# Kernel optimization log

Hardware: AMD Instinct MI355X
Metric: run time of the kernel (lower is better)

The kernel has to match this reference:

```python
import jax, jax.numpy as jnp
import numpy as np

N, H, INTER, M = 8192, 2048, 8192, 2
UP_OUT = 2 * INTER  # gated: up_gate produces interleaved (glu, linear) pairs
EPS = 1e-6
ALPHA = 1.702
LIMIT = 7.0


def setup_inputs() -> dict:
    key = jax.random.key(0)
    k1, k2, k3, k4 = jax.random.split(key, 4)
    x = jax.random.normal(k1, (N, H), dtype=jnp.float32)
    # token stream is pre-permuted so same-modality tokens are contiguous;
    # balanced groups: first N//2 tokens modality 0, rest modality 1
    modality_mapping = jnp.repeat(jnp.arange(M, dtype=jnp.int64), N // M)
    w_norm = jax.random.normal(k2, (H * M,), dtype=jnp.float32) * 0.02
    w_up = jax.random.normal(k3, (UP_OUT * M, H), dtype=jnp.float32) * 0.02
    w_down = jax.random.normal(k4, (H * M, INTER), dtype=jnp.float32) * 0.02
    return {"x": x, "modality_mapping": modality_mapping,
            "w_norm": w_norm, "w_up": w_up, "w_down": w_down}


def reference(x, modality_mapping, w_norm, w_up, w_down):
    # x: [N, H], pre-grouped into M equal contiguous modality chunks.
    n, h = x.shape
    g = n // M  # tokens per modality group
    # ---- MultiModalityRMSNorm (effective weight = 1 + w) ----
    t = x * jax.lax.rsqrt(jnp.mean(x * x, axis=-1, keepdims=True) + EPS)
    tm = t.reshape(M, g, h)                       # [M, g, H]
    tm = tm * (w_norm.reshape(M, 1, h) + 1.0)
    # ---- PackedExpertLinear up_gate: per-modality weight chunk ----
    Wu = w_up.reshape(M, UP_OUT, h)               # [M, 2*INTER, H]
    y = jnp.einsum('mgh,moh->mgo', tm, Wu)        # [M, g, 2*INTER]
    # ---- swiglu7: clamped gated SwiGLU with +1 linear bias ----
    y_glu = jnp.minimum(y[..., ::2], LIMIT)
    y_lin = jnp.clip(y[..., 1::2], -LIMIT, LIMIT)
    a = y_glu * jax.nn.sigmoid(ALPHA * y_glu) * (y_lin + 1.0)  # [M, g, INTER]
    # ---- PackedExpertLinear down_proj ----
    Wd = w_down.reshape(M, h, INTER)              # [M, H, INTER]
    z = jnp.einsum('mgi,mhi->mgh', a, Wd)         # [M, g, H]
    return z.reshape(n, h)
```

## Files before the change

kernel.cpp:

```cpp
#include <hip/hip_runtime.h>
#include <hip/hip_bf16.h>

#define DEVI __device__ __forceinline__

typedef __bf16 bf16x8 __attribute__((ext_vector_type(8)));
typedef float f32x4 __attribute__((ext_vector_type(4)));

namespace {

constexpr int H = 2048;
constexpr int INTER = 8192;
constexpr int M_MOD = 2;
constexpr int N_TOK = 8192;
constexpr int G = N_TOK / M_MOD;
constexpr int UP_OUT = 2 * INTER;

DEVI unsigned short f2bf(float f) {
  unsigned u = __builtin_bit_cast(unsigned, f);
  u += 0x7fffu + ((u >> 16) & 1u);
  return (unsigned short)(u >> 16);
}

DEVI void gload_lds16(const void* g, void* lds) {
  __builtin_amdgcn_global_load_lds(
      (const __attribute__((address_space(1))) unsigned int*)g,
      (__attribute__((address_space(3))) unsigned int*)lds, 16, 0, 0);
}

DEVI void memfence_barrier() {
  asm volatile("" ::: "memory");
  __builtin_amdgcn_s_barrier();
  asm volatile("" ::: "memory");
}

__global__ __launch_bounds__(256) void cvt_f32_bf16(
    const float* __restrict__ in, unsigned short* __restrict__ out, int n4) {
  int idx = blockIdx.x * blockDim.x + threadIdx.x;
  int stride = gridDim.x * blockDim.x;
  for (int i = idx; i < n4; i += stride) {
    float4 v = ((const float4*)in)[i];
    ushort4 o;
    o.x = f2bf(v.x); o.y = f2bf(v.y); o.z = f2bf(v.z); o.w = f2bf(v.w);
    ((ushort4*)out)[i] = o;
  }
}

__global__ __launch_bounds__(256) void rmsnorm_kernel(
    const float* __restrict__ x, const float* __restrict__ w_norm,
    unsigned short* __restrict__ tm) {
  const int row = blockIdx.x;
  const int mod = row >> 12;
  const int t = threadIdx.x;
  const float4* xr = (const float4*)(x + (size_t)row * H);
  const float4* wr = (const float4*)(w_norm + (size_t)mod * H);

  float4 v0 = xr[t];
  float4 v1 = xr[t + 256];
  float ss = v0.x * v0.x + v0.y * v0.y + v0.z * v0.z + v0.w * v0.w +
             v1.x * v1.x + v1.y * v1.y + v1.z * v1.z + v1.w * v1.w;
  #pragma unroll
  for (int o = 32; o > 0; o >>= 1) ss += __shfl_down(ss, o);
  __shared__ float red[4];
  const int w = t >> 6, l = t & 63;
  if (l == 0) red[w] = ss;
  __syncthreads();
  float tot = red[0] + red[1] + red[2] + red[3];
  float rn = rsqrtf(tot * (1.0f / H) + 1e-6f);

  float4 w0 = wr[t];
  float4 w1 = wr[t + 256];
  ushort4 o0, o1;
  o0.x = f2bf(v0.x * rn * (1.f + w0.x));
  o0.y = f2bf(v0.y * rn * (1.f + w0.y));
  o0.z = f2bf(v0.z * rn * (1.f + w0.z));
  o0.w = f2bf(v0.w * rn * (1.f + w0.w));
  o1.x = f2bf(v1.x * rn * (1.f + w1.x));
  o1.y = f2bf(v1.y * rn * (1.f + w1.y));
  o1.z = f2bf(v1.z * rn * (1.f + w1.z));
  o1.w = f2bf(v1.w * rn * (1.f + w1.w));
  ushort4* tr = (ushort4*)(tm + (size_t)row * H);
  tr[t] = o0;
  tr[t + 256] = o1;
}

template <int K, int CT_PER_MOD, int EPI>
__global__ __launch_bounds__(512, 2) void gemm8p(
    const unsigned short* __restrict__ A0, const unsigned short* __restrict__ B0,
    void* __restrict__ O0, long sAm, long sBm, long sOm) {
  __shared__ __align__(16) char smem[2][2][32768];

  constexpr int NT = K / 64;
  constexpr int HMAX = 4 * NT;
  constexpr int NITER = NT / 2;
  constexpr int PER_MOD = 16 * CT_PER_MOD;
  constexpr int NWG = 2 * PER_MOD;
  constexpr int CPX = NWG / 8;

  const int bid0 = blockIdx.x;
  const int bid = (bid0 % 8) * CPX + bid0 / 8;
  const int mod = bid / PER_MOD;
  const int q = bid % PER_MOD;
  const int ct = q / 16;
  const int rt = q % 16;

  const unsigned short* A = A0 + (long)mod * sAm;
  const unsigned short* B = B0 + (long)mod * sBm;

  const int t = threadIdx.x;
  const int w = t >> 6;
  const int l = t & 63;
  const int wr = w >> 2;
  const int wc = w & 3;

  const int fr = l & 15;
  const int fk = l >> 4;
  const int frx = (fr & 7) << 4;

  const unsigned short* gArow = A + (size_t)rt * 256 * K;
  const unsigned short* gBrow = B + (size_t)ct * 256 * K;
  const int srow = t >> 3;
  const int scol = ((t & 7) ^ (srow & 7)) * 8;

  auto stage = [&](int h) {
    if (h >= HMAX) h -= HMAX;
    const int tt = h >> 2, qq = h & 3;
    const int isB = qq >> 1, half = qq & 1, buf = tt & 1;
    const unsigned short* src = (isB ? gBrow : gArow) +
        (size_t)(half * 128 + srow) * K + tt * 64 + scol;
    char* dst = smem[buf][isB] + half * 16384 + t * 16;
    gload_lds16(src, dst);
    gload_lds16(src + (size_t)64 * K, dst + 8192);
  };

  auto rdA = [&](const char* base, int mi, int ks) -> bf16x8 {
    const int row = wr * 128 + mi * 16 + fr;
    return *(const bf16x8*)(base + row * 128 + ((((ks << 2) + fk) << 4) ^ frx));
  };
  auto rdB = [&](const char* base, int ni, int ks) -> bf16x8 {
    const int row = wc * 64 + ni * 16 + fr;
    return *(const bf16x8*)(base + row * 128 + ((((ks << 2) + fk) << 4) ^ frx));
  };

  f32x4 acc[8][4];
  #pragma unroll
  for (int m = 0; m < 8; ++m)
    #pragma unroll
    for (int n = 0; n < 4; ++n) acc[m][n] = (f32x4){0.f, 0.f, 0.f, 0.f};

  bf16x8 a[4][2], b[4][2];

#define MFMAQ(MLO, NLO)                                                       \
  __builtin_amdgcn_s_setprio(1);                                              \
  _Pragma("unroll") for (int ks = 0; ks < 2; ++ks)                            \
  _Pragma("unroll") for (int mi = 0; mi < 4; ++mi)                            \
  _Pragma("unroll") for (int ni = 0; ni < 2; ++ni)                            \
    acc[(MLO) + mi][(NLO) + ni] = __builtin_amdgcn_mfma_f32_16x16x32_bf16(    \
        a[mi][ks], b[(NLO) + ni][ks], acc[(MLO) + mi][(NLO) + ni], 0, 0, 0);  \
  __builtin_amdgcn_s_setprio(0);

  stage(0); stage(1); stage(2); stage(3); stage(4);
  asm volatile("s_waitcnt vmcnt(2)" ::: "memory");
  memfence_barrier();

  const char* A0b = smem[0][0];
  const char* B0b = smem[0][1];
  const char* A1b = smem[1][0];
  const char* B1b = smem[1][1];

  for (int i = 0; i < NITER; ++i) {
    const int h0 = 8 * i;
    #pragma unroll
    for (int mi = 0; mi < 4; ++mi)
      #pragma unroll
      for (int ks = 0; ks < 2; ++ks) a[mi][ks] = rdA(A0b, mi, ks);
    #pragma unroll
    for (int ni = 0; ni < 2; ++ni)
      #pragma unroll
      for (int ks = 0; ks < 2; ++ks) b[ni][ks] = rdB(B0b, ni, ks);
    stage(h0 + 5);
    memfence_barrier();
    MFMAQ(0, 0);
    memfence_barrier();
    #pragma unroll
    for (int ni = 2; ni < 4; ++ni)
      #pragma unroll
      for (int ks = 0; ks < 2; ++ks) b[ni][ks] = rdB(B0b, ni, ks);
    stage(h0 + 6);
    memfence_barrier();
    MFMAQ(0, 2);
    memfence_barrier();
    #pragma unroll
    for (int mi = 0; mi < 4; ++mi)
      #pragma unroll
      for (int ks = 0; ks < 2; ++ks) a[mi][ks] = rdA(A0b, mi + 4, ks);
    stage(h0 + 7);
    memfence_barrier();
    MFMAQ(4, 0);
    memfence_barrier();
    stage(h0 + 8);
    memfence_barrier();
    MFMAQ(4, 2);
    asm volatile("s_waitcnt vmcnt(2)" ::: "memory");
    memfence_barrier();

    #pragma unroll
    for (int mi = 0; mi < 4; ++mi)
      #pragma unroll
      for (int ks = 0; ks < 2; ++ks) a[mi][ks] = rdA(A1b, mi, ks);
    #pragma unroll
    for (int ni = 0; ni < 2; ++ni)
      #pragma unroll
      for (int ks = 0; ks < 2; ++ks) b[ni][ks] = rdB(B1b, ni, ks);
    stage(h0 + 9);
    memfence_barrier();
    MFMAQ(0, 0);
    memfence_barrier();
    #pragma unroll
    for (int ni = 2; ni < 4; ++ni)
      #pragma unroll
      for (int ks = 0; ks < 2; ++ks) b[ni][ks] = rdB(B1b, ni, ks);
    stage(h0 + 10);
    memfence_barrier();
    MFMAQ(0, 2);
    memfence_barrier();
    #pragma unroll
    for (int mi = 0; mi < 4; ++mi)
      #pragma unroll
      for (int ks = 0; ks < 2; ++ks) a[mi][ks] = rdA(A1b, mi + 4, ks);
    stage(h0 + 11);
    memfence_barrier();
    MFMAQ(4, 0);
    memfence_barrier();
    stage(h0 + 12);
    memfence_barrier();
    MFMAQ(4, 2);
    asm volatile("s_waitcnt vmcnt(2)" ::: "memory");
    memfence_barrier();
  }
#undef MFMAQ

  const int row0 = rt * 256 + wr * 128 + (l >> 4) * 4;
  const int col0 = ct * 256 + wc * 64 + (l & 15);
  if (EPI == 0) {
    unsigned short* Oa = (unsigned short*)O0 + (long)mod * sOm;
    #pragma unroll
    for (int m = 0; m < 8; ++m)
      #pragma unroll
      for (int n = 0; n < 4; ++n)
        #pragma unroll
        for (int j = 0; j < 4; ++j) {
          float y = acc[m][n][j];
          float p = __shfl_xor(y, 1);
          if (!(l & 1)) {
            float glu = fminf(y, 7.f);
            float lin = fminf(fmaxf(p, -7.f), 7.f);
            float sg = 1.f / (1.f + __expf(-1.702f * glu));
            float av = glu * sg * (lin + 1.f);
            Oa[(size_t)(row0 + m * 16 + j) * INTER + ((col0 + n * 16) >> 1)] = f2bf(av);
          }
        }
  } else {
    float* Oz = (float*)O0 + (long)mod * sOm;
    #pragma unroll
    for (int m = 0; m < 8; ++m)
      #pragma unroll
      for (int n = 0; n < 4; ++n)
        #pragma unroll
        for (int j = 0; j < 4; ++j)
          Oz[(size_t)(row0 + m * 16 + j) * H + (col0 + n * 16)] = acc[m][n][j];
  }
}

}

extern "C" void kernel_launch(void* const* d_in, const int* in_sizes, int n_in,
                              void* d_out, int out_size, void* d_ws, size_t ws_size,
                              hipStream_t stream) {
  const float* x = (const float*)d_in[0];
  const float* w_norm = (const float*)d_in[2];
  const float* w_up = (const float*)d_in[3];
  const float* w_down = (const float*)d_in[4];

  char* ws = (char*)d_ws;
  unsigned short* wup_bf = (unsigned short*)ws;
  unsigned short* wdn_bf = (unsigned short*)(ws + 134217728L);
  unsigned short* tm = (unsigned short*)(ws + 201326592L);
  unsigned short* abuf = (unsigned short*)(ws + 234881024L);

  cvt_f32_bf16<<<2048, 256, 0, stream>>>(w_up, wup_bf, (UP_OUT * M_MOD * H) / 4);
  cvt_f32_bf16<<<2048, 256, 0, stream>>>(w_down, wdn_bf, (H * M_MOD * INTER) / 4);
  rmsnorm_kernel<<<N_TOK, 256, 0, stream>>>(x, w_norm, tm);

  gemm8p<H, UP_OUT / 256, 0>
      <<<M_MOD * 16 * (UP_OUT / 256), 512, 0, stream>>>(
          tm, wup_bf, abuf, (long)G * H, (long)UP_OUT * H, (long)G * INTER);

  gemm8p<INTER, H / 256, 1>
      <<<M_MOD * 16 * (H / 256), 512, 0, stream>>>(
          abuf, wdn_bf, d_out, (long)G * INTER, (long)H * INTER, (long)G * H);
}
```

Before: 885.9 us.

## Restructure GEMM main loop into k-slice quadrants with reordered async staging

The inner loop now splits each LDS tile by k-slice instead of by N-half. It loads 4 A and 4 B fragments per k-slice into double register sets so LDS reads overlap MFMA quadrants. The order of global-to-LDS stage issues changes (prologue stages 0-3 and 6, then 4/7, 5, 10 per half) and several barriers are dropped, to shorten sync stalls and hide load latency. The stage index permutation must keep data in the correct buffers before each vmcnt wait, so there is a correctness risk if the slot mapping is misordered.

Result: faster. 852.8 us (-3.7%).

```diff
diff --git a/kernel.cpp b/kernel.cpp
--- a/kernel.cpp
+++ b/kernel.cpp
@@ -147,18 +147,23 @@
     #pragma unroll
     for (int n = 0; n < 4; ++n) acc[m][n] = (f32x4){0.f, 0.f, 0.f, 0.f};
 
-  bf16x8 a[4][2], b[4][2];
-
-#define MFMAQ(MLO, NLO)                                                       \
+  bf16x8 aF[4], aF2[4], bF[4], bF2[4];
+
+#define RDA4(DST, BASE, MLO, KS)                                              \
+  _Pragma("unroll") for (int mi = 0; mi < 4; ++mi)                            \
+      DST[mi] = rdA(BASE, (MLO) + mi, KS);
+#define RDB4(DST, BASE, KS)                                                   \
+  _Pragma("unroll") for (int ni = 0; ni < 4; ++ni) DST[ni] = rdB(BASE, ni, KS);
+#define MFMAQ(AR, BR, MLO)                                                    \
   __builtin_amdgcn_s_setprio(1);                                              \
-  _Pragma("unroll") for (int ks = 0; ks < 2; ++ks)                            \
   _Pragma("unroll") for (int mi = 0; mi < 4; ++mi)                            \
-  _Pragma("unroll") for (int ni = 0; ni < 2; ++ni)                            \
-    acc[(MLO) + mi][(NLO) + ni] = __builtin_amdgcn_mfma_f32_16x16x32_bf16(    \
-        a[mi][ks], b[(NLO) + ni][ks], acc[(MLO) + mi][(NLO) + ni], 0, 0, 0);  \
+  _Pragma("unroll") for (int ni = 0; ni < 4; ++ni)                            \
+    acc[(MLO) + mi][ni] = __builtin_amdgcn_mfma_f32_16x16x32_bf16(            \
+        AR[mi], BR[ni], acc[(MLO) + mi][ni], 0, 0, 0);                        \
   __builtin_amdgcn_s_setprio(0);
 
-  stage(0); stage(1); stage(2); stage(3); stage(4);
+  stage(0); stage(1); stage(2); stage(3);
+  stage(6);
   asm volatile("s_waitcnt vmcnt(2)" ::: "memory");
   memfence_barrier();
 
@@ -169,75 +174,47 @@
 
   for (int i = 0; i < NITER; ++i) {
     const int h0 = 8 * i;
-    #pragma unroll
-    for (int mi = 0; mi < 4; ++mi)
-      #pragma unroll
-      for (int ks = 0; ks < 2; ++ks) a[mi][ks] = rdA(A0b, mi, ks);
-    #pragma unroll
-    for (int ni = 0; ni < 2; ++ni)
-      #pragma unroll
-      for (int ks = 0; ks < 2; ++ks) b[ni][ks] = rdB(B0b, ni, ks);
+    RDA4(aF, A0b, 0, 0);
+    RDB4(bF, B0b, 0);
+    stage(h0 + 4); stage(h0 + 7);
+    RDA4(aF2, A0b, 4, 0);
+    MFMAQ(aF, bF, 0);
+    memfence_barrier();
     stage(h0 + 5);
-    memfence_barrier();
-    MFMAQ(0, 0);
-    memfence_barrier();
-    #pragma unroll
-    for (int ni = 2; ni < 4; ++ni)
-      #pragma unroll
-      for (int ks = 0; ks < 2; ++ks) b[ni][ks] = rdB(B0b, ni, ks);
-    stage(h0 + 6);
-    memfence_barrier();
-    MFMAQ(0, 2);
-    memfence_barrier();
-    #pragma unroll
-    for (int mi = 0; mi < 4; ++mi)
-      #pragma unroll
-      for (int ks = 0; ks < 2; ++ks) a[mi][ks] = rdA(A0b, mi + 4, ks);
-    stage(h0 + 7);
-    memfence_barrier();
-    MFMAQ(4, 0);
-    memfence_barrier();
-    stage(h0 + 8);
-    memfence_barrier();
-    MFMAQ(4, 2);
+    RDA4(aF, A0b, 0, 1);
+    RDB4(bF2, B0b, 1);
+    MFMAQ(aF2, bF, 4);
+    memfence_barrier();
+    RDA4(aF2, A0b, 4, 1);
+    MFMAQ(aF, bF2, 0);
+    memfence_barrier();
+    stage(h0 + 10);
+    MFMAQ(aF2, bF2, 4);
     asm volatile("s_waitcnt vmcnt(2)" ::: "memory");
     memfence_barrier();
 
-    #pragma unroll
-    for (int mi = 0; mi < 4; ++mi)
-      #pragma unroll
-      for (int ks = 0; ks < 2; ++ks) a[mi][ks] = rdA(A1b, mi, ks);
-    #pragma unroll
-    for (int ni = 0; ni < 2; ++ni)
-      #pragma unroll
-      for (int ks = 0; ks < 2; ++ks) b[ni][ks] = rdB(B1b, ni, ks);
+    RDA4(aF, A1b, 0, 0);
+    RDB4(bF, B1b, 0);
+    stage(h0 + 8); stage(h0 + 11);
+    RDA4(aF2, A1b, 4, 0);
+    MFMAQ(aF, bF, 0);
+    memfence_barrier();
     stage(h0 + 9);
-    memfence_barrier();
-    MFMAQ(0, 0);
-    memfence_barrier();
-    #pragma unroll
-    for (int ni = 2; ni < 4; ++ni)
-      #pragma unroll
-      for (int ks = 0; ks < 2; ++ks) b[ni][ks] = rdB(B1b, ni, ks);
-    stage(h0 + 10);
-    memfence_barrier();
-    MFMAQ(0, 2);
-    memfence_barrier();
-    #pragma unroll
-    for (int mi = 0; mi < 4; ++mi)
-      #pragma unroll
-      for (int ks = 0; ks < 2; ++ks) a[mi][ks] = rdA(A1b, mi + 4, ks);
-    stage(h0 + 11);
-    memfence_barrier();
-    MFMAQ(4, 0);
-    memfence_barrier();
-    stage(h0 + 12);
-    memfence_barrier();
-    MFMAQ(4, 2);
+    RDA4(aF, A1b, 0, 1);
+    RDB4(bF2, B1b, 1);
+    MFMAQ(aF2, bF, 4);
+    memfence_barrier();
+    RDA4(aF2, A1b, 4, 1);
+    MFMAQ(aF, bF2, 0);
+    memfence_barrier();
+    stage(h0 + 14);
+    MFMAQ(aF2, bF2, 4);
     asm volatile("s_waitcnt vmcnt(2)" ::: "memory");
     memfence_barrier();
   }
 #undef MFMAQ
+#undef RDA4
+#undef RDB4
 
   const int row0 = rt * 256 + wr * 128 + (l >> 4) * 4;
   const int col0 = ct * 256 + wc * 64 + (l & 15);
```
